# Kernel tuning notes

Measured on AMD Instinct MI355X. Metric: run time of the kernel, lower is better.

Reference implementation:

```python
import jax, jax.numpy as jnp
import numpy as np

TEMPERATURE = 0.07
ALPHA = 0.5
TOP_K = 5
SIGMA = 2.0
SCALES = (1, 2, 4)
CL_WEIGHT = 1.0
EPS = 1e-9
NORM_EPS = 1e-12  # F.normalize default eps


def _multi_scale_diffusion(z, scales=SCALES):
    """Row-stochastic affinity from cosine similarity, averaged matrix powers.
    z: [B,N,D] -> assoc: [B,N,N]. (multi_scale_diffusion was external in the
    original repo; this is the standard formulation.)"""
    zn = z / (jnp.linalg.norm(z, axis=-1, keepdims=True) + NORM_EPS)
    sim = jnp.einsum('bnd,bmd->bnm', zn, zn)          # [B,N,N]
    A = jax.nn.softmax(sim, axis=-1)                   # row-stochastic transition
    acc = jnp.zeros_like(A)
    cur, p = A, 1
    for s in sorted(scales):                           # static, tiny loop
        while p < s:
            cur = jnp.einsum('bnk,bkm->bnm', cur, A)   # A^p
            p += 1
        acc = acc + cur
    return acc / float(len(scales))


def _distance_weight(N, sigma):
    idx = jnp.arange(N, dtype=jnp.float32)
    d = idx[:, None] - idx[None, :]
    return jnp.exp(-(d * d) / (2.0 * sigma * sigma))   # [N,N]


def _half_numerator(scores, cross, strong, ar):
    # scores: [B,N,N] extension scores; cross: exp_sim block [B,N,N];
    # strong: [B,N] strong-positive exp_sim; ar: arange(N)
    vals, idx = jax.lax.top_k(scores, TOP_K)           # [B,N,K]
    gath = jnp.take_along_axis(cross, idx, axis=-1)    # [B,N,K]
    mask = (idx != ar[None, :, None]).astype(scores.dtype)  # skip strong positive
    return strong + (mask * vals * gath).sum(-1)       # [B,N]


def reference(proj_z1, proj_z2):
    B, N, D = proj_z1.shape
    assoc1 = _multi_scale_diffusion(proj_z1)
    assoc2 = _multi_scale_diffusion(proj_z2)
    pw = _distance_weight(N, SIGMA)                    # [N,N]

    z_cat = jnp.concatenate([proj_z1, proj_z2], axis=1)        # [B,2N,D]
    z_cat = z_cat / (jnp.linalg.norm(z_cat, axis=-1, keepdims=True) + NORM_EPS)
    sim = jnp.einsum('bnd,bmd->bnm', z_cat, z_cat)             # [B,2N,2N]
    exp_sim = jnp.exp(sim / TEMPERATURE)

    den = exp_sim.sum(-1) - jnp.diagonal(exp_sim, axis1=1, axis2=2)  # [B,2N]
    ar = jnp.arange(N)

    # rows i < N: positives live in view2 (columns N:2N), extension via assoc2
    scores1 = ALPHA * pw[None] + (1.0 - ALPHA) * assoc2        # [B,N,N]
    cross12 = exp_sim[:, :N, N:]                               # [B,N,N]
    strong1 = jnp.diagonal(cross12, axis1=1, axis2=2)          # exp_sim[i, i+N]
    num1 = _half_numerator(scores1, cross12, strong1, ar)

    # rows i >= N: positives live in view1 (columns 0:N), extension via assoc1
    scores2 = ALPHA * pw[None] + (1.0 - ALPHA) * assoc1
    cross21 = exp_sim[:, N:, :N]
    strong2 = jnp.diagonal(cross21, axis1=1, axis2=2)          # exp_sim[i+N, i]
    num2 = _half_numerator(scores2, cross21, strong2, ar)

    num = jnp.concatenate([num1, num2], axis=1)                # [B,2N]
    loss = -jnp.log(num / (den + EPS) + EPS)
    return CL_WEIGHT * loss.mean()


def setup_inputs() -> dict:
    key = jax.random.key(0)
    k1, k2 = jax.random.split(key)
    B, N, D = 16, 1024, 256
    return {
        'proj_z1': jax.random.normal(k1, (B, N, D), dtype=jnp.float32),
        'proj_z2': jax.random.normal(k2, (B, N, D), dtype=jnp.float32),
    }
```

## Files before the change

### kernel.cpp

```cpp
#include <hip/hip_runtime.h>
#include <cmath>
#include <cstdint>

#define BB 16
#define NN_ 1024
#define DD 256

constexpr float INV_T = 1.0f / 0.07f;

typedef __attribute__((ext_vector_type(8))) short bf16x8;
typedef __attribute__((ext_vector_type(4))) float f32x4;

static __device__ __forceinline__ float b2f(ushort u) {
  union { uint i; float f; } c; c.i = ((uint)u) << 16; return c.f;
}
static __device__ __forceinline__ ushort f2b(float f) {
  union { float f; uint i; } c; c.f = f;
  uint r = c.i + 0x7fffu + ((c.i >> 16) & 1u);
  return (ushort)(r >> 16);
}

static __device__ __forceinline__ void gload16(const void* g, void* l) {
  __builtin_amdgcn_global_load_lds((const __attribute__((address_space(1))) unsigned int*)g,
                                   (__attribute__((address_space(3))) unsigned int*)l, 16, 0, 0);
}

__global__ __launch_bounds__(256) void k_norm(const float* __restrict__ z1, const float* __restrict__ z2,
                                              ushort* __restrict__ znAll, float* __restrict__ vecs) {
  const int row = blockIdx.x;
  const int t = threadIdx.x;
  if (row < 256) vecs[(row << 8) + t] = 0.f;
  const bool second = row >= BB * NN_;
  const float* z = second ? z2 : z1;
  const size_t inBase = (size_t)(second ? row - BB * NN_ : row) * DD + t;
  float v = z[inBase];
  float ss = v * v;
#pragma unroll
  for (int o = 32; o; o >>= 1) ss += __shfl_xor(ss, o);
  __shared__ float par[4];
  if ((t & 63) == 0) par[t >> 6] = ss;
  __syncthreads();
  float tot = par[0] + par[1] + par[2] + par[3];
  znAll[(size_t)row * DD + t] = f2b(v / (sqrtf(tot) + 1e-12f));
}

__global__ __launch_bounds__(256) void k_mega256(const ushort* __restrict__ znAll, ushort* __restrict__ XY,
                                                 float* __restrict__ den1, float* __restrict__ den2,
                                                 float* __restrict__ rsum1, float* __restrict__ rsum2) {
  __shared__ __align__(16) ushort smem[17408];
  ushort (*As)[128][32] = (ushort (*)[128][32])smem;
  ushort (*Bs)[128][32] = (ushort (*)[128][32])(smem + 8192);
  ushort (*tb)[136] = (ushort (*)[136])smem;

  const int t = threadIdx.x;
  const int fid = blockIdx.x;
  const bool isSim = fid < 1152;
  const size_t nzd = (size_t)BB * NN_ * DD;
  int b, row0, col0, m = 0;
  const ushort *baseA, *baseB;
  ushort* C = nullptr;
  float *denR, *denC = nullptr, *rsum = nullptr;
  if (isSim) {
    const int xcd = fid & 7;
    const int j = fid >> 3;
    const int unit = j / 36;
    int rem = j % 36;
    m = unit >> 1;
    b = (xcd << 1) | (unit & 1);
    int r = 0;
#pragma unroll
    for (int q = 0; q < 7; ++q)
      if (rem >= 8 - r) { rem -= 8 - r; ++r; }
    row0 = r << 7;
    col0 = (r + rem) << 7;
    baseA = znAll + (m ? 0 : nzd) + (size_t)b * NN_ * DD;
    baseB = baseA;
    C = XY + (size_t)m * BB * NN_ * NN_ + (size_t)b * NN_ * NN_;
    denR = m ? den1 : den2;
    rsum = m ? rsum1 : rsum2;
  } else {
    const int f2 = fid - 1152;
    const int xcd = f2 & 7;
    const int j = f2 >> 3;
    b = (xcd << 1) | (j >> 6);
    const int jj = j & 63;
    row0 = (jj >> 3) << 7;
    col0 = (jj & 7) << 7;
    baseA = znAll + (size_t)b * NN_ * DD;
    baseB = znAll + nzd + (size_t)b * NN_ * DD;
    denR = den1;
    denC = den2;
  }

  const int lane = t & 63, w = t >> 6;
  const int wr = w >> 1, wc = w & 1;
  const int l15 = lane & 15, slot = lane >> 4;
  const int sRow = lane >> 2;
  const int kg = (lane & 3) ^ ((lane >> 3) & 3);
  const int sCol = kg << 3;
  const ushort* gA0 = baseA + (size_t)(row0 + (w << 5) + sRow) * DD + sCol;
  const ushort* gA1 = gA0 + (size_t)16 * DD;
  const ushort* gB0 = baseB + (size_t)(col0 + (w << 5) + sRow) * DD + sCol;
  const ushort* gB1 = gB0 + (size_t)16 * DD;

  f32x4 acc[4][4];
#pragma unroll
  for (int i = 0; i < 4; ++i)
#pragma unroll
    for (int jx = 0; jx < 4; ++jx)
#pragma unroll
      for (int e = 0; e < 4; ++e) acc[i][jx][e] = 0.f;

  gload16(gA0, &As[0][w << 5][0]);
  gload16(gA1, &As[0][(w << 5) + 16][0]);
  gload16(gB0, &Bs[0][w << 5][0]);
  gload16(gB1, &Bs[0][(w << 5) + 16][0]);
  __syncthreads();

  int cur = 0;
  for (int k0 = 0; k0 < DD; k0 += 32) {
    const int nxt = cur ^ 1;
    if (k0 + 32 < DD) {
      gload16(gA0 + k0 + 32, &As[nxt][w << 5][0]);
      gload16(gA1 + k0 + 32, &As[nxt][(w << 5) + 16][0]);
      gload16(gB0 + k0 + 32, &Bs[nxt][w << 5][0]);
      gload16(gB1 + k0 + 32, &Bs[nxt][(w << 5) + 16][0]);
    }
    bf16x8 af[4], bfv[4];
#pragma unroll
    for (int fr = 0; fr < 4; ++fr) {
      const int r = (wr << 6) + (fr << 4) + l15;
      af[fr] = *(const bf16x8*)&As[cur][r][(slot ^ ((r >> 1) & 3)) << 3];
    }
#pragma unroll
    for (int fc = 0; fc < 4; ++fc) {
      const int r = (wc << 6) + (fc << 4) + l15;
      bfv[fc] = *(const bf16x8*)&Bs[cur][r][(slot ^ ((r >> 1) & 3)) << 3];
    }
#pragma unroll
    for (int fr = 0; fr < 4; ++fr)
#pragma unroll
      for (int fc = 0; fc < 4; ++fc)
        acc[fr][fc] = __builtin_amdgcn_mfma_f32_16x16x32_bf16(af[fr], bfv[fc], acc[fr][fc], 0, 0, 0);
    __syncthreads();
    cur = nxt;
  }

  if (isSim) {
    float colp_d[4] = {0.f, 0.f, 0.f, 0.f};
    float colp_e[4] = {0.f, 0.f, 0.f, 0.f};
#pragma unroll
    for (int fr = 0; fr < 4; ++fr) {
#pragma unroll
      for (int jx = 0; jx < 4; ++jx) {
        const int lrow = (wr << 6) + (fr << 4) + (slot << 2) + jx;
        const int grow = row0 + lrow;
        float rs = 0.f, es = 0.f;
#pragma unroll
        for (int fc = 0; fc < 4; ++fc) {
          const int lcol = (wc << 6) + (fc << 4) + l15;
          const int gcol = col0 + lcol;
          const float v = acc[fr][fc][jx];
          const float ev = expf(v);
          const ushort h = f2b(ev);
          C[(size_t)grow * NN_ + gcol] = h;
          tb[lcol][lrow] = h;
          es += ev;
          colp_e[fc] += ev;
          const float dv = expf(v * INV_T);
          if (grow != gcol) { rs += dv; colp_d[fc] += dv; }
        }
#pragma unroll
        for (int o = 1; o < 16; o <<= 1) { rs += __shfl_xor(rs, o); es += __shfl_xor(es, o); }
        if (l15 == 0) {
          atomicAdd(&denR[(size_t)b * NN_ + grow], rs);
          atomicAdd(&rsum[(size_t)b * NN_ + grow], es);
        }
      }
    }
    if (row0 != col0) {
#pragma unroll
      for (int fc = 0; fc < 4; ++fc) {
        float cd = colp_d[fc], ce = colp_e[fc];
        cd += __shfl_xor(cd, 16); cd += __shfl_xor(cd, 32);
        ce += __shfl_xor(ce, 16); ce += __shfl_xor(ce, 32);
        if (slot == 0) {
          const int gcol = col0 + (wc << 6) + (fc << 4) + l15;
          atomicAdd(&denR[(size_t)b * NN_ + gcol], cd);
          atomicAdd(&rsum[(size_t)b * NN_ + gcol], ce);
        }
      }
      __syncthreads();
#pragma unroll
      for (int rep = 0; rep < 8; ++rep) {
        const int cid = rep * 256 + t;
        const int rr = cid >> 4;
        const int c8 = (cid & 15) << 3;
        *(uint4*)&C[(size_t)(col0 + rr) * NN_ + row0 + c8] = *(const uint4*)&tb[rr][c8];
      }
    }
  } else {
    float colp[4] = {0.f, 0.f, 0.f, 0.f};
#pragma unroll
    for (int fr = 0; fr < 4; ++fr) {
#pragma unroll
      for (int jx = 0; jx < 4; ++jx) {
        const int grow = row0 + (wr << 6) + (fr << 4) + (slot << 2) + jx;
        float rs = 0.f;
#pragma unroll
        for (int fc = 0; fc < 4; ++fc) {
          const float e = expf(acc[fr][fc][jx] * INV_T);
          rs += e;
          colp[fc] += e;
        }
#pragma unroll
        for (int o = 1; o < 16; o <<= 1) rs += __shfl_xor(rs, o);
        if (l15 == 0) atomicAdd(&denR[(size_t)b * NN_ + grow], rs);
      }
    }
#pragma unroll
    for (int fc = 0; fc < 4; ++fc) {
      float cs = colp[fc];
      cs += __shfl_xor(cs, 16);
      cs += __shfl_xor(cs, 32);
      if (slot == 0) atomicAdd(&denC[(size_t)b * NN_ + col0 + (wc << 6) + (fc << 4) + l15], cs);
    }
  }
}

__global__ __launch_bounds__(256) void k_scale(ushort* __restrict__ XY, const float* __restrict__ rsum1,
                                               const float* __restrict__ rsum2) {
  const size_t idx8 = ((size_t)blockIdx.x * 256 + threadIdx.x) << 3;
  const size_t nnn = (size_t)BB * NN_ * NN_;
  const int m = idx8 >= nnn;
  const float* r = m ? rsum1 : rsum2;
  const size_t loc = idx8 - (size_t)m * nnn;
  const int grow = (int)(loc >> 10);
  const int bcol = (int)(loc & 1023);
  const int batch = grow >> 10;
  const float rsi = rsqrtf(r[grow]);
  bf16x8 v = *(const bf16x8*)&XY[idx8];
  const float* rb = r + (batch << 10) + bcol;
  const float4 rc0 = *(const float4*)rb;
  const float4 rc1 = *(const float4*)(rb + 4);
  float rj[8] = {rc0.x, rc0.y, rc0.z, rc0.w, rc1.x, rc1.y, rc1.z, rc1.w};
  bf16x8 o;
#pragma unroll
  for (int e = 0; e < 8; ++e) {
    const float wgt = rsi * rsqrtf(rj[e]);
    o[e] = (short)f2b(b2f((ushort)v[e]) * wgt);
  }
  *(bf16x8*)&XY[idx8] = o;
}

__global__ __launch_bounds__(256) void k_megasq(const ushort* __restrict__ XY, ushort* __restrict__ ZW) {
  __shared__ __align__(16) ushort smem[17408];
  ushort (*As)[128][32] = (ushort (*)[128][32])smem;
  ushort (*Bs)[128][32] = (ushort (*)[128][32])(smem + 8192);
  ushort (*tb)[136] = (ushort (*)[136])smem;

  const int t = threadIdx.x;
  const int fid = blockIdx.x;
  const int xcd = fid & 7;
  const int j = fid >> 3;
  const int unit = j / 36;
  int rem = j % 36;
  const int m = unit >> 1;
  const int b = (xcd << 1) | (unit & 1);
  int r = 0;
#pragma unroll
  for (int q = 0; q < 7; ++q)
    if (rem >= 8 - r) { rem -= 8 - r; ++r; }
  const int row0 = r << 7;
  const int col0 = (r + rem) << 7;

  const size_t nnn = (size_t)BB * NN_ * NN_;
  const ushort* baseA = XY + (size_t)m * nnn + (size_t)b * NN_ * NN_;
  ushort* C = ZW + (size_t)m * nnn + (size_t)b * NN_ * NN_;

  const int lane = t & 63, w = t >> 6;
  const int wr = w >> 1, wc = w & 1;
  const int l15 = lane & 15, slot = lane >> 4;
  const int sRow = lane >> 2;
  const int kg = (lane & 3) ^ ((lane >> 3) & 3);
  const int sCol = kg << 3;
  const ushort* gA0 = baseA + (size_t)(row0 + (w << 5) + sRow) * NN_ + sCol;
  const ushort* gA1 = gA0 + (size_t)16 * NN_;
  const ushort* gB0 = baseA + (size_t)(col0 + (w << 5) + sRow) * NN_ + sCol;
  const ushort* gB1 = gB0 + (size_t)16 * NN_;

  f32x4 acc[4][4];
#pragma unroll
  for (int i = 0; i < 4; ++i)
#pragma unroll
    for (int jx = 0; jx < 4; ++jx)
#pragma unroll
      for (int e = 0; e < 4; ++e) acc[i][jx][e] = 0.f;

  gload16(gA0, &As[0][w << 5][0]);
  gload16(gA1, &As[0][(w << 5) + 16][0]);
  gload16(gB0, &Bs[0][w << 5][0]);
  gload16(gB1, &Bs[0][(w << 5) + 16][0]);
  __syncthreads();

  int cur = 0;
  for (int k0 = 0; k0 < NN_; k0 += 32) {
    const int nxt = cur ^ 1;
    if (k0 + 32 < NN_) {
      gload16(gA0 + k0 + 32, &As[nxt][w << 5][0]);
      gload16(gA1 + k0 + 32, &As[nxt][(w << 5) + 16][0]);
      gload16(gB0 + k0 + 32, &Bs[nxt][w << 5][0]);
      gload16(gB1 + k0 + 32, &Bs[nxt][(w << 5) + 16][0]);
    }
    bf16x8 af[4], bfv[4];
#pragma unroll
    for (int fr = 0; fr < 4; ++fr) {
      const int rr = (wr << 6) + (fr << 4) + l15;
      af[fr] = *(const bf16x8*)&As[cur][rr][(slot ^ ((rr >> 1) & 3)) << 3];
    }
#pragma unroll
    for (int fc = 0; fc < 4; ++fc) {
      const int rr = (wc << 6) + (fc << 4) + l15;
      bfv[fc] = *(const bf16x8*)&Bs[cur][rr][(slot ^ ((rr >> 1) & 3)) << 3];
    }
#pragma unroll
    for (int fr = 0; fr < 4; ++fr)
#pragma unroll
      for (int fc = 0; fc < 4; ++fc)
        acc[fr][fc] = __builtin_amdgcn_mfma_f32_16x16x32_bf16(af[fr], bfv[fc], acc[fr][fc], 0, 0, 0);
    __syncthreads();
    cur = nxt;
  }

#pragma unroll
  for (int fr = 0; fr < 4; ++fr) {
#pragma unroll
    for (int jx = 0; jx < 4; ++jx) {
      const int lrow = (wr << 6) + (fr << 4) + (slot << 2) + jx;
      const int grow = row0 + lrow;
#pragma unroll
      for (int fc = 0; fc < 4; ++fc) {
        const int lcol = (wc << 6) + (fc << 4) + l15;
        const ushort h = f2b(acc[fr][fc][jx]);
        C[(size_t)grow * NN_ + col0 + lcol] = h;
        tb[lcol][lrow] = h;
      }
    }
  }
  if (row0 != col0) {
    __syncthreads();
#pragma unroll
    for (int rep = 0; rep < 8; ++rep) {
      const int cid = rep * 256 + t;
      const int rr = cid >> 4;
      const int c8 = (cid & 15) << 3;
      *(uint4*)&C[(size_t)(col0 + rr) * NN_ + row0 + c8] = *(const uint4*)&tb[rr][c8];
    }
  }
}

__global__ __launch_bounds__(256) void k_megaloss(const ushort* __restrict__ XY, const ushort* __restrict__ ZW,
                                                  const ushort* __restrict__ znAll,
                                                  const float* __restrict__ rsum1, const float* __restrict__ rsum2,
                                                  float* __restrict__ den1, float* __restrict__ den2) {
  const int gid = (blockIdx.x << 2) + (threadIdx.x >> 6);
  const int lane = threadIdx.x & 63;
  const int h = gid >> 14;
  const int lr = gid & 16383;
  const int b = lr >> 10, i = lr & 1023;
  const size_t nnn = (size_t)BB * NN_ * NN_;
  const size_t nzd = (size_t)BB * NN_ * DD;
  const ushort* M = XY + (size_t)h * nnn + (size_t)b * NN_ * NN_;
  const ushort* M2 = ZW + (size_t)h * nnn + (size_t)b * NN_ * NN_;
  const float* r = h ? rsum1 : rsum2;
  float* den = h ? den2 : den1;
  const ushort* znS = znAll + (size_t)h * nzd;
  const ushort* znO = znAll + (size_t)(1 - h) * nzd;
  const int w0 = min(max(i - 2, 0), NN_ - 5);

  const ushort* zr = M2 + (size_t)i * NN_ + (lane << 4);
  const bf16x8 r0 = *(const bf16x8*)zr;
  const bf16x8 r1 = *(const bf16x8*)(zr + 8);

  const ushort4 qv = *(const ushort4*)&znS[((size_t)b * NN_ + i) * DD + (lane << 2)];
  const float q0 = b2f(qv.x), q1 = b2f(qv.y), q2 = b2f(qv.z), q3 = b2f(qv.w);

  float a4[5], cd[5];
#pragma unroll
  for (int s = 0; s < 5; ++s) {
    const int jx = w0 + s;
    float p = 0.f;
    if (jx != i) {
      const ushort* wrp = M2 + (size_t)jx * NN_ + (lane << 4);
      const bf16x8 wv0 = *(const bf16x8*)wrp;
      const bf16x8 wv1 = *(const bf16x8*)(wrp + 8);
#pragma unroll
      for (int e = 0; e < 8; ++e)
        p += b2f((ushort)r0[e]) * b2f((ushort)wv0[e]) + b2f((ushort)r1[e]) * b2f((ushort)wv1[e]);
    }
    const ushort4 ov = *(const ushort4*)&znO[((size_t)b * NN_ + jx) * DD + (lane << 2)];
    float c = q0 * b2f(ov.x) + q1 * b2f(ov.y) + q2 * b2f(ov.z) + q3 * b2f(ov.w);
#pragma unroll
    for (int o = 32; o; o >>= 1) { p += __shfl_xor(p, o); c += __shfl_xor(c, o); }
    a4[s] = p;
    cd[s] = c;
  }

  const float rsi = rsqrtf(r[(size_t)b * NN_ + i]);
  float num = 0.f;
#pragma unroll
  for (int s = 0; s < 5; ++s) {
    const int jx = w0 + s;
    const float g = expf(cd[s] * INV_T);
    if (jx == i) {
      num += g;
    } else {
      const float d = (float)(jx - i);
      const float pw = expf(-d * d * 0.125f);
      const float ratio = sqrtf(r[(size_t)b * NN_ + jx]) * rsi;
      const float mband = b2f(M[(size_t)i * NN_ + jx]);
      const float m2band = b2f(M2[(size_t)i * NN_ + jx]);
      const float sc = 0.5f * pw + ratio * (mband + m2band + a4[s]) * (0.5f / 3.0f);
      num += sc * g;
    }
  }

  if (lane == 0) {
    const float dn = den[(size_t)b * NN_ + i];
    den[(size_t)b * NN_ + i] = -logf(num / (dn + 1e-9f) + 1e-9f);
  }
}

__global__ __launch_bounds__(256) void k_final(const float* __restrict__ lossRows, float* __restrict__ out) {
  const int t = threadIdx.x;
  float s = 0.f;
  for (int idx = t; idx < BB * 2 * NN_; idx += 256) s += lossRows[idx];
#pragma unroll
  for (int o = 32; o; o >>= 1) s += __shfl_xor(s, o);
  __shared__ float p[4];
  if ((t & 63) == 0) p[t >> 6] = s;
  __syncthreads();
  if (t == 0) out[0] = (p[0] + p[1] + p[2] + p[3]) / (float)(BB * 2 * NN_);
}

extern "C" void kernel_launch(void* const* d_in, const int* in_sizes, int n_in, void* d_out, int out_size,
                              void* d_ws, size_t ws_size, hipStream_t stream) {
  const float* z1 = (const float*)d_in[0];
  const float* z2 = (const float*)d_in[1];
  float* out = (float*)d_out;

  const size_t nzd = (size_t)BB * NN_ * DD;
  const size_t nnn = (size_t)BB * NN_ * NN_;
  const size_t nv = (size_t)BB * NN_;

  ushort* znAll = (ushort*)d_ws;
  ushort* XY = znAll + 2 * nzd;
  ushort* ZW = XY + 2 * nnn;
  float* den1 = (float*)(ZW + 2 * nnn);
  float* den2 = den1 + nv;
  float* rsum1 = den2 + nv;
  float* rsum2 = rsum1 + nv;

  const size_t needed = 2 * nzd * 2 + 4 * nnn * 2 + 4 * nv * 4;
  if (ws_size < needed) return;

  dim3 blk(256);

  k_norm<<<2 * BB * NN_, blk, 0, stream>>>(z1, z2, znAll, den1);

  k_mega256<<<1152 + 1024, blk, 0, stream>>>(znAll, XY, den1, den2, rsum1, rsum2);

  k_scale<<<(int)(2 * nnn / 2048), blk, 0, stream>>>(XY, rsum1, rsum2);

  k_megasq<<<1152, blk, 0, stream>>>(XY, ZW);

  k_megaloss<<<(int)(2 * nv / 4), blk, 0, stream>>>(XY, ZW, znAll, rsum1, rsum2, den1, den2);

  k_final<<<1, blk, 0, stream>>>(den1, out);
}
```

Before: 296.4 us.

## Vectorize norm kernel, use fast exp intrinsics, remap loss block order

The normalization kernel now gives each wavefront one row, reading float4 and writing ushort4, which removes the shared-memory reduction and the block barrier and launches a quarter as many blocks. The accurate expf calls in the similarity and loss kernels become __expf intrinsics to cut transcendental cost. The loss kernel's block index is permuted so that consecutive blocks land on different parts of the data, probably to spread them across XCDs or memory channels. The fast exp lowers precision somewhat, and exp(v/0.07) relies on it staying accurate at large arguments.

New measurement: 269.1 us. 9.2% less time.

```diff
diff --git a/kernel.cpp b/kernel.cpp
--- a/kernel.cpp
+++ b/kernel.cpp
@@ -27,21 +27,20 @@
 
 __global__ __launch_bounds__(256) void k_norm(const float* __restrict__ z1, const float* __restrict__ z2,
                                               ushort* __restrict__ znAll, float* __restrict__ vecs) {
-  const int row = blockIdx.x;
-  const int t = threadIdx.x;
-  if (row < 256) vecs[(row << 8) + t] = 0.f;
+  if (blockIdx.x < 256) vecs[(blockIdx.x << 8) + threadIdx.x] = 0.f;
+  const int row = (blockIdx.x << 2) + (threadIdx.x >> 6);
+  const int lane = threadIdx.x & 63;
   const bool second = row >= BB * NN_;
   const float* z = second ? z2 : z1;
-  const size_t inBase = (size_t)(second ? row - BB * NN_ : row) * DD + t;
-  float v = z[inBase];
-  float ss = v * v;
+  const size_t rbase = (size_t)(second ? row - BB * NN_ : row) * DD;
+  const float4 v = ((const float4*)(z + rbase))[lane];
+  float ss = v.x * v.x + v.y * v.y + v.z * v.z + v.w * v.w;
 #pragma unroll
   for (int o = 32; o; o >>= 1) ss += __shfl_xor(ss, o);
-  __shared__ float par[4];
-  if ((t & 63) == 0) par[t >> 6] = ss;
-  __syncthreads();
-  float tot = par[0] + par[1] + par[2] + par[3];
-  znAll[(size_t)row * DD + t] = f2b(v / (sqrtf(tot) + 1e-12f));
+  const float inv = 1.0f / (sqrtf(ss) + 1e-12f);
+  ushort4 o4;
+  o4.x = f2b(v.x * inv); o4.y = f2b(v.y * inv); o4.z = f2b(v.z * inv); o4.w = f2b(v.w * inv);
+  ((ushort4*)(znAll + (size_t)row * DD))[lane] = o4;
 }
 
 __global__ __launch_bounds__(256) void k_mega256(const ushort* __restrict__ znAll, ushort* __restrict__ XY,
@@ -161,13 +160,13 @@
           const int lcol = (wc << 6) + (fc << 4) + l15;
           const int gcol = col0 + lcol;
           const float v = acc[fr][fc][jx];
-          const float ev = expf(v);
+          const float ev = __expf(v);
           const ushort h = f2b(ev);
           C[(size_t)grow * NN_ + gcol] = h;
           tb[lcol][lrow] = h;
           es += ev;
           colp_e[fc] += ev;
-          const float dv = expf(v * INV_T);
+          const float dv = __expf(v * INV_T);
           if (grow != gcol) { rs += dv; colp_d[fc] += dv; }
         }
 #pragma unroll
@@ -209,7 +208,7 @@
         float rs = 0.f;
 #pragma unroll
         for (int fc = 0; fc < 4; ++fc) {
-          const float e = expf(acc[fr][fc][jx] * INV_T);
+          const float e = __expf(acc[fr][fc][jx] * INV_T);
           rs += e;
           colp[fc] += e;
         }
@@ -363,7 +362,9 @@
                                                   const ushort* __restrict__ znAll,
                                                   const float* __restrict__ rsum1, const float* __restrict__ rsum2,
                                                   float* __restrict__ den1, float* __restrict__ den2) {
-  const int gid = (blockIdx.x << 2) + (threadIdx.x >> 6);
+  const int fid = blockIdx.x;
+  const int blk = ((fid & 7) << 10) | (fid >> 3);
+  const int gid = (blk << 2) + (threadIdx.x >> 6);
   const int lane = threadIdx.x & 63;
   const int h = gid >> 14;
   const int lr = gid & 16383;
@@ -411,12 +412,12 @@
 #pragma unroll
   for (int s = 0; s < 5; ++s) {
     const int jx = w0 + s;
-    const float g = expf(cd[s] * INV_T);
+    const float g = __expf(cd[s] * INV_T);
     if (jx == i) {
       num += g;
     } else {
       const float d = (float)(jx - i);
-      const float pw = expf(-d * d * 0.125f);
+      const float pw = __expf(-d * d * 0.125f);
       const float ratio = sqrtf(r[(size_t)b * NN_ + jx]) * rsi;
       const float mband = b2f(M[(size_t)i * NN_ + jx]);
       const float m2band = b2f(M2[(size_t)i * NN_ + jx]);
@@ -466,7 +467,7 @@
 
   dim3 blk(256);
 
-  k_norm<<<2 * BB * NN_, blk, 0, stream>>>(z1, z2, znAll, den1);
+  k_norm<<<(2 * BB * NN_) / 4, blk, 0, stream>>>(z1, z2, znAll, den1);
 
   k_mega256<<<1152 + 1024, blk, 0, stream>>>(znAll, XY, den1, den2, rsum1, rsum2);
 
```
